# Performance work log

Hardware: AMD Instinct MI355X
Metric: run time of the kernel (lower is better)

## Reference

```python
import jax, jax.numpy as jnp
import numpy as np

NUM_FEAT = 64        # per-head dim == input channel C
HIDDEN = 1024        # total hidden size
NUM_HEADS = HIDDEN // NUM_FEAT  # 16


def setup_inputs() -> dict:
    key = jax.random.key(0)
    k1, k2, k3, k4, k5 = jax.random.split(key, 5)
    B, N, C = 4, 2048, NUM_FEAT
    hidden_states = jax.random.normal(k1, (B, N, C), dtype=jnp.float32)
    # nn.Linear(num_feat, hidden*3): weight [3*hidden, num_feat], store transposed for x @ W
    s_qkv = 1.0 / np.sqrt(C)
    qkv_w = jax.random.uniform(k2, (C, 3 * HIDDEN), jnp.float32, -s_qkv, s_qkv)
    qkv_b = jax.random.uniform(k3, (3 * HIDDEN,), jnp.float32, -s_qkv, s_qkv)
    s_out = 1.0 / np.sqrt(HIDDEN)
    out_w = jax.random.uniform(k4, (HIDDEN, C), jnp.float32, -s_out, s_out)
    out_b = jax.random.uniform(k5, (C,), jnp.float32, -s_out, s_out)
    return {"hidden_states": hidden_states, "qkv_w": qkv_w, "qkv_b": qkv_b,
            "out_w": out_w, "out_b": out_b}


def reference(hidden_states, qkv_w, qkv_b, out_w, out_b):
    B, N, C = hidden_states.shape
    H, D = NUM_HEADS, NUM_FEAT  # head count, head dim
    # qkv projection: [B,N,3*HIDDEN] -> [3,B,H,N,D]
    qkv = hidden_states @ qkv_w + qkv_b
    qkv = qkv.reshape(B, N, 3, H, D).transpose(2, 0, 3, 1, 4)
    q, k, v = qkv[0], qkv[1], qkv[2]
    # scaled dot-product attention with materialized scores (faithful to source)
    scores = jnp.einsum('bhqd,bhkd->bhqk', q, k) / jnp.sqrt(jnp.float32(D))
    probs = jax.nn.softmax(scores, axis=-1)
    ctx = jnp.einsum('bhqk,bhkd->bhqd', probs, v)           # [B,H,N,D]
    ctx = ctx.transpose(0, 2, 1, 3).reshape(B, N, H * D)    # [B,N,HIDDEN]
    out = ctx @ out_w + out_b                               # [B,N,C]
    return jax.nn.gelu(out, approximate=False)
```

## Files before the change

### kernel.cpp

```cpp
#include <hip/hip_runtime.h>
#include <math.h>

#define B_ 4
#define N_ 2048
#define C_ 64
#define H_ 16
#define D_ 64
#define HID 1024

#define QSCALE 0.18033688011112042f

typedef short bf16x8 __attribute__((ext_vector_type(8)));
typedef unsigned short u16x8 __attribute__((ext_vector_type(8)));
typedef float f32x4 __attribute__((ext_vector_type(4)));

#define MFMA(a, b, c) __builtin_amdgcn_mfma_f32_16x16x32_bf16((a), (b), (c), 0, 0, 0)

typedef __attribute__((address_space(3))) void lds_t;
typedef const __attribute__((address_space(1))) void gbl_t;
#define ASYNC16(g, l) __builtin_amdgcn_global_load_lds((gbl_t*)(g), (lds_t*)(l), 16, 0, 0)

static __device__ __forceinline__ unsigned short f2bf(float f) {
  unsigned u = __float_as_uint(f);
  u += 0x7FFFu + ((u >> 16) & 1u);
  return (unsigned short)(u >> 16);
}
static __device__ __forceinline__ float bf2f(unsigned short h) {
  return __uint_as_float((unsigned)h << 16);
}
static __device__ __forceinline__ unsigned pkbf(float a, float b) {
  return __builtin_amdgcn_perm(__float_as_uint(b), __float_as_uint(a),
                               0x07060302u);
}

__global__ __launch_bounds__(256, 2) void qkv_kernel(
    const float* __restrict__ X, const float* __restrict__ W,
    const float* __restrict__ bias, const float* __restrict__ W2,
    unsigned short* __restrict__ Qhi, unsigned short* __restrict__ Khi,
    unsigned short* __restrict__ Vhi,
    unsigned short* __restrict__ W2THi, unsigned short* __restrict__ W2TLo) {
  const int t = threadIdx.x;
  const int ct = blockIdx.x;
  const int tt = blockIdx.y;

  if (ct == 24) {
    int idx0 = tt * 1024 + t * 4;
#pragma unroll
    for (int e = 0; e < 4; ++e) {
      int idx = idx0 + e;
      int k = idx & 1023, col = idx >> 10;
      float v = W2[(size_t)k * 64 + col];
      unsigned short hi = f2bf(v);
      W2THi[(size_t)col * 1024 + k] = hi;
      W2TLo[(size_t)col * 1024 + k] = f2bf(v - bf2f(hi));
    }
    return;
  }

  __shared__ unsigned short qsmem[32768];
  unsigned short* sXhi = qsmem;
  unsigned short* sXlo = qsmem + 8192;
  unsigned short* sWhi = qsmem + 16384;
  unsigned short* sWlo = qsmem + 24576;

  {
    const int kg = t & 7, r0 = t >> 3;
#pragma unroll
    for (int i = 0; i < 4; ++i) {
      int row = r0 + i * 32;
      const float* src = &X[(size_t)(tt * 128 + row) * 64 + kg * 8];
      f32x4 a = *(const f32x4*)src;
      f32x4 b = *(const f32x4*)(src + 4);
      u16x8 hi8, lo8;
#pragma unroll
      for (int j = 0; j < 4; ++j) {
        hi8[j] = f2bf(a[j]);
        lo8[j] = f2bf(a[j] - bf2f(hi8[j]));
        hi8[4 + j] = f2bf(b[j]);
        lo8[4 + j] = f2bf(b[j] - bf2f(hi8[4 + j]));
      }
      int off = row * 64 + ((kg ^ (row & 7)) << 3);
      *(u16x8*)&sXhi[off] = hi8;
      *(u16x8*)&sXlo[off] = lo8;
    }
  }
  {
    const int col = t & 127, kg0 = t >> 7;
#pragma unroll
    for (int i = 0; i < 4; ++i) {
      int kg = kg0 + i * 2;
      u16x8 hi8, lo8;
#pragma unroll
      for (int j = 0; j < 8; ++j) {
        float v = W[(size_t)(kg * 8 + j) * 3072 + ct * 128 + col];
        unsigned short h = f2bf(v);
        hi8[j] = h;
        lo8[j] = f2bf(v - bf2f(h));
      }
      int off = col * 64 + ((kg ^ (col & 7)) << 3);
      *(u16x8*)&sWhi[off] = hi8;
      *(u16x8*)&sWlo[off] = lo8;
    }
  }
  __syncthreads();

  const int w = t >> 6, lane = t & 63;
  const int lid = lane & 15, quad = lane >> 4;

  bf16x8 xa[2][2][2];
#pragma unroll
  for (int mt = 0; mt < 2; ++mt) {
    int row = w * 32 + mt * 16 + lid;
#pragma unroll
    for (int kc = 0; kc < 2; ++kc) {
      int off = row * 64 + (((kc * 4 + quad) ^ (row & 7)) << 3);
      xa[mt][kc][0] = *(const bf16x8*)&sXhi[off];
      xa[mt][kc][1] = *(const bf16x8*)&sXlo[off];
    }
  }

  f32x4 acc[2][8];
#pragma unroll
  for (int mt = 0; mt < 2; ++mt)
#pragma unroll
    for (int nt = 0; nt < 8; ++nt) acc[mt][nt] = (f32x4){0.f, 0.f, 0.f, 0.f};

#pragma unroll
  for (int nt = 0; nt < 8; ++nt) {
    int col = nt * 16 + lid;
#pragma unroll
    for (int kc = 0; kc < 2; ++kc) {
      int boff = col * 64 + (((kc * 4 + quad) ^ (col & 7)) << 3);
      bf16x8 wbh = *(const bf16x8*)&sWhi[boff];
      bf16x8 wbl = *(const bf16x8*)&sWlo[boff];
#pragma unroll
      for (int mt = 0; mt < 2; ++mt) {
        f32x4 c = acc[mt][nt];
        c = MFMA(xa[mt][kc][0], wbh, c);
        c = MFMA(xa[mt][kc][0], wbl, c);
        c = MFMA(xa[mt][kc][1], wbh, c);
        acc[mt][nt] = c;
      }
    }
  }

  __syncthreads();

  const int s = ct >> 3;
  const float scale = (s == 0) ? QSCALE : 1.0f;
  float bias_r[8];
#pragma unroll
  for (int nt = 0; nt < 8; ++nt) bias_r[nt] = bias[ct * 128 + nt * 16 + lid];

  if (s < 2) {
    unsigned short(*sOut)[136] = (unsigned short(*)[136])qsmem;
#pragma unroll
    for (int mt = 0; mt < 2; ++mt)
#pragma unroll
      for (int nt = 0; nt < 8; ++nt) {
        f32x4 v = acc[mt][nt];
#pragma unroll
        for (int r = 0; r < 4; ++r)
          sOut[w * 32 + mt * 16 + quad * 4 + r][nt * 16 + lid] =
              f2bf((v[r] + bias_r[nt]) * scale);
      }
    __syncthreads();
    const int ltok = t >> 1, half = t & 1;
    const int token = tt * 128 + ltok;
    const int bb = token >> 11, n = token & 2047;
    const int head = (ct * 2 + half) & 15;
    unsigned short* A = (s == 0) ? Qhi : Khi;
    size_t dst = ((size_t)(bb * H_ + head) * N_ + n) * D_;
    const unsigned short* srcr = &sOut[ltok][half * 64];
#pragma unroll
    for (int j = 0; j < 8; ++j)
      *(uint4*)&A[dst + j * 8] = *(const uint4*)&srcr[j * 8];
  } else {
    unsigned short(*sT)[136] = (unsigned short(*)[136])qsmem;
#pragma unroll
    for (int mt = 0; mt < 2; ++mt)
#pragma unroll
      for (int nt = 0; nt < 8; ++nt) {
        f32x4 v = acc[mt][nt];
        unsigned short h0 = f2bf(v[0] + bias_r[nt]);
        unsigned short h1 = f2bf(v[1] + bias_r[nt]);
        unsigned short h2 = f2bf(v[2] + bias_r[nt]);
        unsigned short h3 = f2bf(v[3] + bias_r[nt]);
        uint2 dw;
        dw.x = (unsigned)h0 | ((unsigned)h1 << 16);
        dw.y = (unsigned)h2 | ((unsigned)h3 << 16);
        *(uint2*)&sT[nt * 16 + lid][w * 32 + mt * 16 + quad * 4] = dw;
      }
    __syncthreads();
    const int col = t >> 1, half = t & 1;
    const int hv = (ct & 7) * 2 + (col >> 6), d = col & 63;
    const int bbv = tt >> 4;
    const int n0 = (tt & 15) * 128 + half * 64;
    size_t row = (size_t)((bbv * H_ + hv) * D_ + d);
    unsigned short* dstp = Vhi + row * (size_t)N_ + n0;
    const unsigned short* srcr = &sT[col][half * 64];
#pragma unroll
    for (int j = 0; j < 8; ++j)
      *(uint4*)(dstp + j * 8) = *(const uint4*)&srcr[j * 8];
  }
}

__global__ __launch_bounds__(256, 4) void attn_kernel(
    const unsigned short* __restrict__ Qhi, const unsigned short* __restrict__ Khi,
    const unsigned short* __restrict__ VThi,
    unsigned short* __restrict__ ctxHi, unsigned short* __restrict__ ctxLo) {
  __shared__ unsigned short smem[16384];

  const int tid = threadIdx.x;
  const int w = tid >> 6, lane = tid & 63;
  const int lid = lane & 15, quad = lane >> 4;
  const int l7 = lid & 7;
  unsigned short* sK = smem;
  unsigned short* sVt = smem + 6144;
  unsigned short* sP = smem + 12288 + w * 1024;

  const int id = blockIdx.x;
  const int bh = id & 63;
  const int qt = id >> 6;
  const int b = bh >> 4, h = bh & 15;
  const size_t base = (size_t)bh * N_ * D_;
  const int row0 = qt * 128 + w * 32;

  bf16x8 qh[2][2];
#pragma unroll
  for (int mt = 0; mt < 2; ++mt) {
    int row = row0 + mt * 16 + lid;
    const unsigned short* qph = Qhi + base + (size_t)row * D_;
#pragma unroll
    for (int kc = 0; kc < 2; ++kc)
      qh[mt][kc] = *(const bf16x8*)(qph + kc * 32 + quad * 8);
  }

  f32x4 o[2][4];
  float lacc[2] = {0.f, 0.f};
#pragma unroll
  for (int mt = 0; mt < 2; ++mt)
#pragma unroll
    for (int dnt = 0; dnt < 4; ++dnt) o[mt][dnt] = (f32x4){0.f, 0.f, 0.f, 0.f};

  const int lrow = lane >> 3;
  const int lgr = (lane & 7) ^ lrow;

  auto stage = [&](int kt_, int buf_) {
    size_t gk = base + (size_t)(kt_ * 32 + w * 8 + lrow) * 64 + lgr * 8;
    ASYNC16(Khi + gk, sK + buf_ * 2048 + (w * 8) * 64);
    int pr = w * 8 + lrow;
    int vd = pr * 2 + (lgr >> 2);
    int vk0 = (lgr & 3) * 8;
    size_t gv = base + (size_t)vd * N_ + kt_ * 32 + vk0;
    ASYNC16(VThi + gv, sVt + buf_ * 2048 + (w * 8) * 64);
  };

  const int NT = N_ / 32;
  stage(0, 0);
  stage(1, 1);

  int cur = 0;
  for (int kt = 0; kt < NT; ++kt) {
    if (kt < NT - 1)
      asm volatile("s_waitcnt vmcnt(2)" ::: "memory");
    else
      asm volatile("s_waitcnt vmcnt(0)" ::: "memory");
    __builtin_amdgcn_s_barrier();
    __builtin_amdgcn_sched_barrier(0);
    if (kt + 2 < NT) {
      int nxt2 = cur >= 1 ? cur - 1 : cur + 2;
      stage(kt + 2, nxt2);
    }
    const int buf = cur;

    f32x4 sc[2][2];
    __builtin_amdgcn_s_setprio(1);
#pragma unroll
    for (int nt = 0; nt < 2; ++nt) {
      int key = nt * 16 + lid;
#pragma unroll
      for (int kc = 0; kc < 2; ++kc) {
        int off = key * 64 + (((kc * 4 + quad) ^ l7) << 3);
        bf16x8 kh_ = *(const bf16x8*)&sK[buf * 2048 + off];
#pragma unroll
        for (int mt = 0; mt < 2; ++mt) {
          f32x4 c = (kc == 0) ? (f32x4){0.f, 0.f, 0.f, 0.f} : sc[mt][nt];
          c = MFMA(kh_, qh[mt][kc], c);
          sc[mt][nt] = c;
        }
      }
    }
    __builtin_amdgcn_s_setprio(0);

    bf16x8 pa[2];
#pragma unroll
    for (int mt = 0; mt < 2; ++mt) {
      float lsum = 0.f;
#pragma unroll
      for (int nt = 0; nt < 2; ++nt) {
        float p0 = __builtin_amdgcn_exp2f(sc[mt][nt][0]);
        float p1 = __builtin_amdgcn_exp2f(sc[mt][nt][1]);
        float p2 = __builtin_amdgcn_exp2f(sc[mt][nt][2]);
        float p3 = __builtin_amdgcn_exp2f(sc[mt][nt][3]);
        lsum += (p0 + p1) + (p2 + p3);
        uint2 dw;
        dw.x = pkbf(p0, p1);
        dw.y = pkbf(p2, p3);
        int idx = (mt * 8 + (lid >> 1)) * 64 +
                  (((nt * 2 + (quad >> 1) + 4 * (lid & 1)) ^ ((lid >> 1) & 7))
                   << 3) +
                  (quad & 1) * 4;
        *(uint2*)&sP[idx] = dw;
      }
      lsum += __shfl_xor(lsum, 16);
      lsum += __shfl_xor(lsum, 32);
      lacc[mt] += lsum;
      int ridx = (mt * 8 + (lid >> 1)) * 64 +
                 (((quad + 4 * (lid & 1)) ^ ((lid >> 1) & 7)) << 3);
      pa[mt] = *(const bf16x8*)&sP[ridx];
    }

    __builtin_amdgcn_s_setprio(1);
#pragma unroll
    for (int dnt = 0; dnt < 4; ++dnt) {
      int voff = buf * 2048 + (dnt * 8 + (lid >> 1)) * 64 +
                 (((quad + (lid & 1) * 4) ^ ((lid >> 1) & 7)) << 3);
      bf16x8 vh = *(const bf16x8*)&sVt[voff];
#pragma unroll
      for (int mt = 0; mt < 2; ++mt) o[mt][dnt] = MFMA(vh, pa[mt], o[mt][dnt]);
    }
    __builtin_amdgcn_s_setprio(0);

    cur = cur == 2 ? 0 : cur + 1;
  }

  __syncthreads();
  float* scr = (float*)smem + w * 1088;
  const int erow = lane >> 2, ecq = lane & 3;
#pragma unroll
  for (int mt = 0; mt < 2; ++mt) {
    float inv = 1.0f / lacc[mt];
#pragma unroll
    for (int dnt = 0; dnt < 4; ++dnt) {
      f32x4 v = o[mt][dnt] * inv;
      *(f32x4*)&scr[lid * 68 + dnt * 16 + quad * 4] = v;
    }
    int token = b * N_ + row0 + mt * 16 + erow;
    size_t doff = (size_t)token * HID + h * 64;
#pragma unroll
    for (int i = 0; i < 4; ++i) {
      f32x4 v4 = *(const f32x4*)&scr[erow * 68 + ecq * 4 + i * 16];
      unsigned short hi_[4], lo_[4];
#pragma unroll
      for (int j = 0; j < 4; ++j) {
        hi_[j] = f2bf(v4[j]);
        lo_[j] = f2bf(v4[j] - bf2f(hi_[j]));
      }
      uint2 hw, lw;
      hw.x = (unsigned)hi_[0] | ((unsigned)hi_[1] << 16);
      hw.y = (unsigned)hi_[2] | ((unsigned)hi_[3] << 16);
      lw.x = (unsigned)lo_[0] | ((unsigned)lo_[1] << 16);
      lw.y = (unsigned)lo_[2] | ((unsigned)lo_[3] << 16);
      *(uint2*)&ctxHi[doff + ecq * 4 + i * 16] = hw;
      *(uint2*)&ctxLo[doff + ecq * 4 + i * 16] = lw;
    }
  }
}

__global__ __launch_bounds__(256) void out_kernel(
    const unsigned short* __restrict__ ctxHi, const unsigned short* __restrict__ ctxLo,
    const unsigned short* __restrict__ W2THi, const unsigned short* __restrict__ W2TLo,
    const float* __restrict__ b2, float* __restrict__ out) {
  __shared__ float sO[4][4][16][16];
  const int tid = threadIdx.x;
  const int w = tid >> 6, lane = tid & 63;
  const int lid = lane & 15, quad = lane >> 4;
  const int tok0 = blockIdx.x * 16;

  f32x4 acc[4];
#pragma unroll
  for (int nt = 0; nt < 4; ++nt) acc[nt] = (f32x4){0.f, 0.f, 0.f, 0.f};

  const size_t abase = (size_t)(tok0 + lid) * HID + w * 256 + quad * 8;

  for (int kc = 0; kc < 8; ++kc) {
    bf16x8 ah = *(const bf16x8*)&ctxHi[abase + kc * 32];
    bf16x8 al = *(const bf16x8*)&ctxLo[abase + kc * 32];
#pragma unroll
    for (int nt = 0; nt < 4; ++nt) {
      size_t boff =
          (size_t)(nt * 16 + lid) * HID + w * 256 + kc * 32 + quad * 8;
      bf16x8 bh = *(const bf16x8*)&W2THi[boff];
      bf16x8 bl = *(const bf16x8*)&W2TLo[boff];
      f32x4 c = acc[nt];
      c = MFMA(ah, bh, c);
      c = MFMA(ah, bl, c);
      c = MFMA(al, bh, c);
      acc[nt] = c;
    }
  }

#pragma unroll
  for (int nt = 0; nt < 4; ++nt)
#pragma unroll
    for (int r = 0; r < 4; ++r) sO[w][nt][quad * 4 + r][lid] = acc[nt][r];
  __syncthreads();

  const int col = tid & 63;
  const int nt = col >> 4, cl = col & 15;
#pragma unroll
  for (int rr = 0; rr < 4; ++rr) {
    int row = w * 4 + rr;
    float v = sO[0][nt][row][cl] + sO[1][nt][row][cl] + sO[2][nt][row][cl] +
              sO[3][nt][row][cl] + b2[col];
    float g = 0.5f * v * (1.0f + erff(v * 0.70710678118654752f));
    out[(size_t)(tok0 + row) * 64 + col] = g;
  }
}

extern "C" void kernel_launch(void* const* d_in, const int* in_sizes, int n_in,
                              void* d_out, int out_size, void* d_ws, size_t ws_size,
                              hipStream_t stream) {
  const float* X = (const float*)d_in[0];
  const float* qkv_w = (const float*)d_in[1];
  const float* qkv_b = (const float*)d_in[2];
  const float* out_w = (const float*)d_in[3];
  const float* out_b = (const float*)d_in[4];
  float* out = (float*)d_out;

  const size_t NE = (size_t)B_ * H_ * N_ * D_;
  unsigned short* ws16 = (unsigned short*)d_ws;
  unsigned short* Qhi = ws16 + 0 * NE;
  unsigned short* Khi = ws16 + 1 * NE;
  unsigned short* VThi = ws16 + 2 * NE;
  unsigned short* ctxHi = ws16 + 3 * NE;
  unsigned short* ctxLo = ws16 + 4 * NE;
  unsigned short* W2THi = ws16 + 5 * NE;
  unsigned short* W2TLo = W2THi + 65536;

  qkv_kernel<<<dim3(25, 64), 256, 0, stream>>>(X, qkv_w, qkv_b, out_w, Qhi,
                                               Khi, VThi, W2THi, W2TLo);
  attn_kernel<<<1024, 256, 0, stream>>>(Qhi, Khi, VThi, ctxHi, ctxLo);
  out_kernel<<<512, 256, 0, stream>>>(ctxHi, ctxLo, W2THi, W2TLo, out_b, out);
}
```

Baseline: 201.1 us.

## Load K tiles directly from global into registers instead of via LDS

K tiles now go straight from global memory into registers, double-buffered across two register sets with the loop unrolled by two. They no longer pass through asynchronous LDS copies followed by swizzled LDS reads. This drops the K region of shared memory, which shrinks LDS use per block and could allow more resident blocks, and it also removes the LDS read traffic for K. In exchange it raises register pressure, adds uncoalesced-ish per-lane global loads whose latency must be hidden, and requires the vmcnt waits to be retuned to account for the extra outstanding loads.

```diff
diff --git a/kernel.cpp b/kernel.cpp
--- a/kernel.cpp
+++ b/kernel.cpp
@@ -209,15 +209,13 @@
     const unsigned short* __restrict__ Qhi, const unsigned short* __restrict__ Khi,
     const unsigned short* __restrict__ VThi,
     unsigned short* __restrict__ ctxHi, unsigned short* __restrict__ ctxLo) {
-  __shared__ unsigned short smem[16384];
+  __shared__ unsigned short smem[10240];
 
   const int tid = threadIdx.x;
   const int w = tid >> 6, lane = tid & 63;
   const int lid = lane & 15, quad = lane >> 4;
-  const int l7 = lid & 7;
-  unsigned short* sK = smem;
-  unsigned short* sVt = smem + 6144;
-  unsigned short* sP = smem + 12288 + w * 1024;
+  unsigned short* sVt = smem;
+  unsigned short* sP = smem + 6144 + w * 1024;
 
   const int id = blockIdx.x;
   const int bh = id & 63;
@@ -247,8 +245,6 @@
   const int lgr = (lane & 7) ^ lrow;
 
   auto stage = [&](int kt_, int buf_) {
-    size_t gk = base + (size_t)(kt_ * 32 + w * 8 + lrow) * 64 + lgr * 8;
-    ASYNC16(Khi + gk, sK + buf_ * 2048 + (w * 8) * 64);
     int pr = w * 8 + lrow;
     int vd = pr * 2 + (lgr >> 2);
     int vk0 = (lgr & 3) * 8;
@@ -256,42 +252,44 @@
     ASYNC16(VThi + gv, sVt + buf_ * 2048 + (w * 8) * 64);
   };
 
+  auto loadK = [&](int kt_, bf16x8 (&kh)[2][2]) {
+#pragma unroll
+    for (int nt = 0; nt < 2; ++nt)
+#pragma unroll
+      for (int kc = 0; kc < 2; ++kc)
+        kh[nt][kc] =
+            *(const bf16x8*)&Khi[base + (size_t)(kt_ * 32 + nt * 16 + lid) * 64 +
+                                 kc * 32 + quad * 8];
+  };
+
   const int NT = N_ / 32;
-  stage(0, 0);
-  stage(1, 1);
-
-  int cur = 0;
-  for (int kt = 0; kt < NT; ++kt) {
+
+  auto ibody = [&](int kt, bf16x8 (&kh)[2][2], int buf) {
     if (kt < NT - 1)
-      asm volatile("s_waitcnt vmcnt(2)" ::: "memory");
+      asm volatile("s_waitcnt vmcnt(5)" ::: "memory");
     else
       asm volatile("s_waitcnt vmcnt(0)" ::: "memory");
     __builtin_amdgcn_s_barrier();
     __builtin_amdgcn_sched_barrier(0);
     if (kt + 2 < NT) {
-      int nxt2 = cur >= 1 ? cur - 1 : cur + 2;
+      int nxt2 = buf >= 1 ? buf - 1 : buf + 2;
       stage(kt + 2, nxt2);
     }
-    const int buf = cur;
 
     f32x4 sc[2][2];
     __builtin_amdgcn_s_setprio(1);
 #pragma unroll
-    for (int nt = 0; nt < 2; ++nt) {
-      int key = nt * 16 + lid;
-#pragma unroll
-      for (int kc = 0; kc < 2; ++kc) {
-        int off = key * 64 + (((kc * 4 + quad) ^ l7) << 3);
-        bf16x8 kh_ = *(const bf16x8*)&sK[buf * 2048 + off];
+    for (int nt = 0; nt < 2; ++nt)
+#pragma unroll
+      for (int kc = 0; kc < 2; ++kc)
 #pragma unroll
         for (int mt = 0; mt < 2; ++mt) {
           f32x4 c = (kc == 0) ? (f32x4){0.f, 0.f, 0.f, 0.f} : sc[mt][nt];
-          c = MFMA(kh_, qh[mt][kc], c);
-          sc[mt][nt] = c;
+          sc[mt][nt] = MFMA(kh[nt][kc], qh[mt][kc], c);
         }
-      }
-    }
     __builtin_amdgcn_s_setprio(0);
+
+    if (kt + 2 < NT) loadK(kt + 2, kh);
 
     bf16x8 pa[2];
 #pragma unroll
@@ -331,8 +329,20 @@
       for (int mt = 0; mt < 2; ++mt) o[mt][dnt] = MFMA(vh, pa[mt], o[mt][dnt]);
     }
     __builtin_amdgcn_s_setprio(0);
-
-    cur = cur == 2 ? 0 : cur + 1;
+  };
+
+  bf16x8 khA[2][2], khB[2][2];
+  stage(0, 0);
+  loadK(0, khA);
+  stage(1, 1);
+  loadK(1, khB);
+
+  int cur = 0;
+  for (int kt = 0; kt < NT; kt += 2) {
+    ibody(kt, khA, cur);
+    int cur1 = cur == 2 ? 0 : cur + 1;
+    ibody(kt + 1, khB, cur1);
+    cur = cur1 == 2 ? 0 : cur1 + 1;
   }
 
   __syncthreads();
```

Result: slower. 252.4 us (+25.5%).
